# Performance work log

Hardware: AMD Instinct MI355X
Metric: run time of the kernel (lower is better)

Reference implementation:

```python
import jax, jax.numpy as jnp
import numpy as np
from jax import lax

T_D = 0.7          # condensation radius
T_B = 0.2          # min beta to seed a condensate
FEATURE_LENGTH = 9 # columns of raw features before the prediction block
N_FEAT = 17        # n_ccoords = N_FEAT - 14 = 3
N_EVENTS = 16
POINTS_PER_EVENT = 65536


def setup_inputs() -> dict:
    key = jax.random.key(0)
    N = N_EVENTS * POINTS_PER_EVENT
    # uniform [0,1): betas in [0,1), ccoords in the unit cube -> realistic clustering
    x = jax.random.uniform(key, (N, N_FEAT), dtype=jnp.float32)
    row_splits = (jnp.arange(N_EVENTS + 1) * POINTS_PER_EVENT).astype(jnp.int32)
    return {"x": x, "row_splits": row_splits}


def _build_condensates(ccoords, betas, radius, min_beta):
    """Greedy NMS-like condensation, vectorized over events.
    ccoords: [E, P, C] float; betas: [E, P] float.
    Returns asso [E,P] int32 (index of assigned condensate, -1 = noise) and
    iscond [E,P] bool (condensation point flags).
    """
    E, P, _ = ccoords.shape
    r2 = radius * radius

    def masked_beta(asso):
        return jnp.where(asso < 0, betas, -1.0)

    def cond_fn(state):
        asso, _ = state
        return jnp.any(jnp.max(masked_beta(asso), axis=1) >= min_beta)

    def body_fn(state):
        asso, iscond = state
        mb = masked_beta(asso)                     # [E,P]
        ref = jnp.argmax(mb, axis=1)               # [E] highest-beta unassigned point
        valid = jnp.take_along_axis(mb, ref[:, None], axis=1)[:, 0] >= min_beta  # [E]
        refc = jnp.take_along_axis(ccoords, ref[:, None, None], axis=1)          # [E,1,C]
        distsq = jnp.sum((ccoords - refc) ** 2, axis=-1)                          # [E,P]
        assign = (asso < 0) & (distsq <= r2) & valid[:, None]
        asso = jnp.where(assign, ref[:, None].astype(jnp.int32), asso)
        newcond = (jnp.arange(P)[None, :] == ref[:, None]) & valid[:, None]
        return asso, iscond | newcond

    asso0 = jnp.full((E, P), -1, dtype=jnp.int32)
    iscond0 = jnp.zeros((E, P), dtype=jnp.bool_)
    return lax.while_loop(cond_fn, body_fn, (asso0, iscond0))


def reference(x, row_splits):
    E = row_splits.shape[0] - 1
    N, F = x.shape
    P = N // E  # uniform events (RaggedConstructTensor equivalent for equal splits)
    n_ccoords = F - 14
    x_pred = x[:, FEATURE_LENGTH:]
    n_pred = x_pred.shape[-1]
    betas = x_pred[:, 0].reshape(E, P)
    ccoords = x_pred[:, n_pred - n_ccoords:].reshape(E, P, n_ccoords)

    asso, iscond = _build_condensates(ccoords, betas, T_D, T_B)

    ncond = jnp.sum(iscond, axis=1).astype(jnp.int32)  # condensates per event
    out_row_splits = jnp.concatenate(
        [jnp.zeros((1,), jnp.int32), jnp.cumsum(ncond).astype(jnp.int32)])
    # jit-safe equivalent of dout = x[iscond > 0]: zero-mask non-condensates
    mask = iscond.reshape(-1, 1).astype(x.dtype)
    dout = x * mask  # [N, F], rows of non-condensates are zero
    return dout, out_row_splits
```

## Files before the change

kernel.cpp:

```cpp
#include <hip/hip_runtime.h>

typedef unsigned long long u64;
typedef unsigned int u32;
typedef float f4n __attribute__((ext_vector_type(4)));

static constexpr int NF = 17;
static constexpr int BCOL = 9;
static constexpr int CCOL = 14;
static constexpr int RPB = 512;
static constexpr int CHUNK = 4096;
static constexpr int REFCAP = 64;
static constexpr int SCAP = 8192;
static constexpr int BPE = 32;
static constexpr int WCHK = 8;

#define T_B_F ((float)0.2)
#define R2_F  ((float)(0.7*0.7))

__device__ __forceinline__ u64 shfl_down_u64(u64 v, int off){
    u32 lo = (u32)v, hi = (u32)(v >> 32);
    lo = __shfl_down(lo, off, 64);
    hi = __shfl_down(hi, off, 64);
    return ((u64)hi << 32) | lo;
}

__device__ __forceinline__ float dist2(float cx, float cy, float cz,
                                       float rx, float ry, float rz){
    #pragma clang fp contract(off)
    float dx = cx - rx, dy = cy - ry, dz = cz - rz;
    float sx = dx * dx, sy = dy * dy, sz = dz * dz;
    return (sx + sy) + sz;
}

__device__ __forceinline__ u64 makeKey(float beta, u32 idx){
    return ((u64)__float_as_uint(beta) << 32) | (u64)(0xFFFFFFFFu - idx);
}

__device__ __forceinline__ int bucketOf(float b){
    int v = (int)((b - 0.2f) * 320.0f);
    return v > 255 ? 255 : v;
}

__device__ __forceinline__ void blockArgmax(u64 bk, int bs,
                                            u64* wkey, int* wslot,
                                            u64* skey, int* sslot){
    int tid = threadIdx.x, lid = tid & 63, wid = tid >> 6;
    #pragma unroll
    for (int off = 32; off > 0; off >>= 1){
        u64 ok = shfl_down_u64(bk, off);
        int os = __shfl_down(bs, off, 64);
        if (ok > bk){ bk = ok; bs = os; }
    }
    if (lid == 0){ wkey[wid] = bk; wslot[wid] = bs; }
    __syncthreads();
    if (wid == 0){
        u64 k2 = (lid < 16) ? wkey[lid] : 0;
        int s2 = (lid < 16) ? wslot[lid] : -1;
        #pragma unroll
        for (int off = 8; off > 0; off >>= 1){
            u64 ok = shfl_down_u64(k2, off);
            int os = __shfl_down(s2, off, 64);
            if (ok > k2){ k2 = ok; s2 = os; }
        }
        if (lid == 0){ *skey = k2; *sslot = s2; }
    }
    __syncthreads();
}

__device__ int lds_nms_fast(float4* cp, float* cb, int* ci, int m,
                            u64* wkey, int* wslot, u64* skey, int* sslot,
                            float4* refs_xyz, int* refs_idx, int refbase, int nref)
{
    int tid = threadIdx.x;
    u64 bk = 0; int bs = -1;
    for (int k = tid; k < m; k += 1024){
        u64 kk = makeKey(cb[k], (u32)ci[k]);
        if (kk > bk){ bk = kk; bs = k; }
    }
    blockArgmax(bk, bs, wkey, wslot, skey, sslot);
    while (*skey != 0){
        int rs = *sslot;
        float4 rv = cp[rs];
        if (tid == 0 && nref < REFCAP){
            refs_xyz[refbase + nref] = rv;
            refs_idx[refbase + nref] = ci[rs];
        }
        nref++;
        bk = 0; bs = -1;
        for (int k = tid; k < m; k += 1024){
            float b = cb[k];
            if (b >= 0.f){
                float4 p = cp[k];
                if (dist2(p.x, p.y, p.z, rv.x, rv.y, rv.z) <= R2_F) cb[k] = -1.f;
                else { u64 kk = makeKey(b, (u32)ci[k]); if (kk > bk){ bk = kk; bs = k; } }
            }
        }
        blockArgmax(bk, bs, wkey, wslot, skey, sslot);
    }
    return nref;
}

__global__ void k_init(u32* ws){
    for (int i = threadIdx.x; i < 4352; i += 1024) ws[i] = 0;
}

__global__ __launch_bounds__(256) void k_main(
    const float4* __restrict__ x4, f4n* __restrict__ out4, int n4out,
    int* __restrict__ cnt, int* __restrict__ hist,
    float4* __restrict__ cand_xyz, int* __restrict__ cand_idx,
    int P, int chunksPerEvent, int filterBlocks)
{
    __shared__ float4 lrow[RPB];
    __shared__ int lh[256];
    __shared__ int swc[4], swb[4], sbase;

    int b = blockIdx.x;
    if (b >= filterBlocks){
        int i = (b - filterBlocks) * 256 + threadIdx.x;
        int stride = (gridDim.x - filterBlocks) * 256;
        f4n z = {0.f, 0.f, 0.f, 0.f};
        for (; i < n4out; i += stride) __builtin_nontemporal_store(z, &out4[i]);
        return;
    }
    int e = b / chunksPerEvent;
    int chunk = b % chunksPerEvent;
    int rowStart = chunk * RPB;
    size_t tile4 = (size_t)b * (RPB * NF / 4);
    int tid = threadIdx.x;
    lh[tid] = 0;

    const int N4 = RPB * NF / 4;
    for (int i = tid; i < N4; i += 256){
        float4 v = x4[tile4 + i];
        float vv[4] = {v.x, v.y, v.z, v.w};
        int f0 = 4 * i;
        #pragma unroll
        for (int j = 0; j < 4; j++){
            int flat = f0 + j;
            int row = flat / NF;
            int col = flat - row * NF;
            if (col == BCOL)       ((float*)&lrow[row])[3] = vv[j];
            else if (col >= CCOL)  ((float*)&lrow[row])[col - CCOL] = vv[j];
        }
    }
    __syncthreads();

    int lid = tid & 63, wid = tid >> 6;
    float4 a0 = lrow[tid], a1 = lrow[tid + 256];
    bool k0 = (a0.w >= T_B_F), k1 = (a1.w >= T_B_F);
    u64 bal0 = __ballot(k0), bal1 = __ballot(k1);
    int wcnt = __popcll(bal0) + __popcll(bal1);
    if (k0) atomicAdd(&lh[bucketOf(a0.w)], 1);
    if (k1) atomicAdd(&lh[bucketOf(a1.w)], 1);
    if (lid == 0) swc[wid] = wcnt;
    __syncthreads();
    if (tid == 0){
        int tot = 0;
        for (int w = 0; w < 4; w++){ swb[w] = tot; tot += swc[w]; }
        sbase = tot ? atomicAdd(&cnt[e], tot) : 0;
    }
    __syncthreads();
    int base = sbase + swb[wid];
    u64 lm = (1ull << lid) - 1;
    size_t eoff = (size_t)e * P;
    if (k0){
        int pos = base + __popcll(bal0 & lm);
        cand_xyz[eoff + pos] = a0;
        cand_idx[eoff + pos] = rowStart + tid;
    }
    if (k1){
        int pos = base + __popcll(bal0) + __popcll(bal1 & lm);
        cand_xyz[eoff + pos] = a1;
        cand_idx[eoff + pos] = rowStart + tid + 256;
    }
    if (lh[tid]) atomicAdd(&hist[e * 256 + tid], lh[tid]);
}

__global__ __launch_bounds__(256) void k_gather(
    const int* __restrict__ hist, const float4* __restrict__ cand_xyz,
    const int* __restrict__ cand_idx, const int* __restrict__ cnt,
    float4* __restrict__ top_xyz, int* __restrict__ top_idx,
    int* __restrict__ topcnt, int* __restrict__ cutoffB, int P)
{
    __shared__ int lh[256];
    __shared__ int swc[4], swb[4], sbase, scut;
    int e = blockIdx.x / BPE, c = blockIdx.x % BPE;
    int tid = threadIdx.x;
    lh[tid] = hist[e * 256 + tid];
    __syncthreads();
    if (tid == 0){
        int tot = 0, cu = 0;
        for (int bb = 255; bb >= 0; bb--){
            if (tot + lh[bb] > CHUNK){ cu = bb + 1; break; }
            tot += lh[bb];
        }
        scut = cu;
        if (c == 0) cutoffB[e] = cu;
    }
    __syncthreads();
    int cut = scut, n = cnt[e];
    int lid = tid & 63, wid = tid >> 6;
    size_t eoff = (size_t)e * P;
    int stride = BPE * 256;

    float4 cc[WCHK]; int ix[WCHK]; bool kp[WCHK]; u64 bal[WCHK];
    int wcnt = 0;
    #pragma unroll
    for (int k = 0; k < WCHK; k++){
        int i = c * 256 + tid + k * stride;
        bool inb = i < n;
        int ii = inb ? i : 0;
        float4 v = cand_xyz[eoff + ii];
        kp[k] = inb && (bucketOf(v.w) >= cut);
        cc[k] = v;
        bal[k] = __ballot(kp[k]);
        wcnt += __popcll(bal[k]);
        ix[k] = kp[k] ? cand_idx[eoff + ii] : 0;
    }
    if (lid == 0) swc[wid] = wcnt;
    __syncthreads();
    if (tid == 0){
        int tot = 0;
        for (int w = 0; w < 4; w++){ swb[w] = tot; tot += swc[w]; }
        sbase = tot ? atomicAdd(&topcnt[e], tot) : 0;
    }
    __syncthreads();
    int pos = sbase + swb[wid];
    u64 lm = (1ull << lid) - 1;
    #pragma unroll
    for (int k = 0; k < WCHK; k++){
        if (kp[k]){
            int p_ = pos + __popcll(bal[k] & lm);
            top_xyz[e * CHUNK + p_] = cc[k];
            top_idx[e * CHUNK + p_] = ix[k];
        }
        pos += __popcll(bal[k]);
    }
}

__global__ __launch_bounds__(1024) void k_nms1(
    const float4* __restrict__ top_xyz, const int* __restrict__ top_idx,
    const int* __restrict__ topcnt,
    float4* __restrict__ refs_xyz, int* __restrict__ refs_idx,
    int* __restrict__ nref1)
{
    __shared__ float4 cp[CHUNK];
    __shared__ float cb[CHUNK];
    __shared__ int ci[CHUNK];
    __shared__ u64 wkey[16]; __shared__ int wslot[16];
    __shared__ u64 skey; __shared__ int sslot;

    int e = blockIdx.x, tid = threadIdx.x;
    int m = topcnt[e]; if (m > CHUNK) m = CHUNK;
    for (int i = tid; i < m; i += 1024){
        float4 v = top_xyz[e * CHUNK + i];
        cp[i] = v; cb[i] = v.w; ci[i] = top_idx[e * CHUNK + i];
    }
    __syncthreads();
    int nref = lds_nms_fast(cp, cb, ci, m, wkey, wslot, &skey, &sslot,
                            refs_xyz, refs_idx, e * REFCAP, 0);
    if (tid == 0) nref1[e] = nref;
}

__global__ __launch_bounds__(256) void k_suppress(
    const float4* __restrict__ cand_xyz, const int* __restrict__ cand_idx,
    const int* __restrict__ cnt, const float4* __restrict__ refs_xyz,
    const int* __restrict__ nref1, const int* __restrict__ cutoffB,
    float4* __restrict__ surv_xyz, int* __restrict__ surv_idx,
    int* __restrict__ survcnt, int P)
{
    __shared__ float4 lref[REFCAP];
    __shared__ int swc[4], swb[4], sbase;
    int e = blockIdx.x / BPE, c = blockIdx.x % BPE;
    int nr = nref1[e]; if (nr > REFCAP) nr = REFCAP;
    int cut = cutoffB[e], n = cnt[e];
    for (int i = threadIdx.x; i < nr; i += 256) lref[i] = refs_xyz[e * REFCAP + i];
    __syncthreads();
    int tid = threadIdx.x, lid = tid & 63, wid = tid >> 6;
    size_t eoff = (size_t)e * P;
    int stride = BPE * 256;

    float4 cc[WCHK]; int ix[WCHK]; bool kp[WCHK]; u64 bal[WCHK];
    int wcnt = 0;
    #pragma unroll
    for (int k = 0; k < WCHK; k++){
        int i = c * 256 + tid + k * stride;
        bool inb = i < n;
        int ii = inb ? i : 0;
        float4 v = cand_xyz[eoff + ii];
        bool keep = inb && (bucketOf(v.w) < cut);
        if (keep){
            for (int r = 0; r < nr; r++){
                float4 rf = lref[r];
                if (dist2(v.x, v.y, v.z, rf.x, rf.y, rf.z) <= R2_F){ keep = false; break; }
            }
        }
        cc[k] = v; kp[k] = keep;
        bal[k] = __ballot(keep);
        wcnt += __popcll(bal[k]);
        ix[k] = keep ? cand_idx[eoff + ii] : 0;
    }
    if (lid == 0) swc[wid] = wcnt;
    __syncthreads();
    if (tid == 0){
        int tot = 0;
        for (int w = 0; w < 4; w++){ swb[w] = tot; tot += swc[w]; }
        sbase = tot ? atomicAdd(&survcnt[e], tot) : 0;
    }
    __syncthreads();
    int pos = sbase + swb[wid];
    u64 lm = (1ull << lid) - 1;
    size_t soff = (size_t)e * SCAP;
    #pragma unroll
    for (int k = 0; k < WCHK; k++){
        if (kp[k]){
            int p_ = pos + __popcll(bal[k] & lm);
            if (p_ < SCAP){ surv_xyz[soff + p_] = cc[k]; surv_idx[soff + p_] = ix[k]; }
        }
        pos += __popcll(bal[k]);
    }
}

__global__ __launch_bounds__(1024) void k_nms2(
    const float* __restrict__ x, float* __restrict__ out,
    const float4* __restrict__ surv_xyz, const int* __restrict__ surv_idx,
    const int* __restrict__ survcnt,
    float4* __restrict__ scr_xyz, int* __restrict__ scr_idx,
    float4* __restrict__ refs_xyz, int* __restrict__ refs_idx,
    const int* __restrict__ nref1,
    int* __restrict__ ncond, int* __restrict__ done, int P, int E)
{
    __shared__ float4 cp[CHUNK];
    __shared__ float cb[CHUNK];
    __shared__ int ci[CHUNK];
    __shared__ u64 wkey[16]; __shared__ int wslot[16];
    __shared__ u64 skey; __shared__ int sslot;
    __shared__ int scnt2, sLast;

    int e = blockIdx.x, tid = threadIdx.x, lid = tid & 63, wid = tid >> 6;
    int m = survcnt[e]; if (m > SCAP) m = SCAP;
    size_t soff = (size_t)e * SCAP;
    int nref = nref1[e]; if (nref > REFCAP) nref = REFCAP;

    const float4* sx = surv_xyz + soff;
    const int* si = surv_idx + soff;
    float4* fbx[2] = {scr_xyz + (size_t)e * P, scr_xyz + (size_t)e * P + SCAP};
    int* fbi[2] = {scr_idx + (size_t)e * P, scr_idx + (size_t)e * P + SCAP};
    int pp = 0;

    while (m > CHUNK){
        u64 bk = 0; int bs = -1;
        for (int i = tid; i < m; i += 1024){
            float4 v = sx[i];
            u64 kk = makeKey(v.w, (u32)si[i]);
            if (kk > bk){ bk = kk; bs = i; }
        }
        blockArgmax(bk, bs, wkey, wslot, &skey, &sslot);
        if (tid == 0) scnt2 = 0;
        __syncthreads();
        float4 rv = sx[sslot];
        if (tid == 0 && nref < REFCAP){
            refs_xyz[e * REFCAP + nref] = rv;
            refs_idx[e * REFCAP + nref] = si[sslot];
        }
        nref++;
        __syncthreads();
        for (int i0 = 0; i0 < m; i0 += 1024){
            int i = i0 + tid;
            bool keep = false; float4 v = make_float4(0.f,0.f,0.f,0.f); int id_ = 0;
            if (i < m){
                v = sx[i]; id_ = si[i];
                keep = !(dist2(v.x, v.y, v.z, rv.x, rv.y, rv.z) <= R2_F);
            }
            u64 bal = __ballot(keep);
            int cw = __popcll(bal);
            int b_ = 0;
            if (lid == 0) b_ = cw ? atomicAdd(&scnt2, cw) : 0;
            b_ = __shfl(b_, 0, 64);
            if (keep){
                int p_ = b_ + __popcll(bal & ((1ull << lid) - 1));
                fbx[pp][p_] = v; fbi[pp][p_] = id_;
            }
        }
        __syncthreads();
        m = scnt2;
        sx = fbx[pp]; si = fbi[pp]; pp ^= 1;
        __syncthreads();
    }

    for (int i = tid; i < m; i += 1024){
        float4 v = sx[i];
        cp[i] = v; cb[i] = v.w; ci[i] = si[i];
    }
    __syncthreads();
    nref = lds_nms_fast(cp, cb, ci, m, wkey, wslot, &skey, &sslot,
                        refs_xyz, refs_idx, e * REFCAP, nref);
    if (nref > REFCAP) nref = REFCAP;

    for (int i = tid; i < nref * NF; i += 1024){
        int j = i / NF, f = i - j * NF;
        int row = refs_idx[e * REFCAP + j];
        size_t b = ((size_t)e * P + row) * NF;
        out[b + f] = x[b + f];
    }
    if (tid == 0) atomicExch(&ncond[e], nref);
    __threadfence();
    __syncthreads();
    if (tid == 0) sLast = atomicAdd(done, 1);
    __syncthreads();
    if (sLast == E - 1 && tid == 0){
        size_t so = (size_t)E * P * NF;
        int s = 0;
        out[so] = 0.f;
        for (int i = 0; i < E; i++){
            s += atomicAdd(&ncond[i], 0);
            out[so + i + 1] = (float)s;
        }
    }
}

extern "C" void kernel_launch(void* const* d_in, const int* in_sizes, int n_in,
                              void* d_out, int out_size, void* d_ws, size_t ws_size,
                              hipStream_t stream) {
    const float* x = (const float*)d_in[0];
    int N = in_sizes[0] / NF;
    int E = in_sizes[1] - 1;
    int P = N / E;
    float* out = (float*)d_out;
    char* ws = (char*)d_ws;

    int* cnt     = (int*)(ws + 0);
    int* survcnt = (int*)(ws + 64);
    int* ncond   = (int*)(ws + 128);
    int* done    = (int*)(ws + 192);
    int* nref1   = (int*)(ws + 256);
    int* cutoffB = (int*)(ws + 320);
    int* topcnt  = (int*)(ws + 384);
    int* hist    = (int*)(ws + 1024);
    float4* refs_xyz = (float4*)(ws + 20480);
    int* refs_idx    = (int*)(ws + 36864);
    float4* top_xyz  = (float4*)(ws + 65536);
    int* top_idx     = (int*)(ws + 65536 + (size_t)E*CHUNK*16);
    size_t o = 65536 + (size_t)E*CHUNK*20;
    float4* cand_xyz = (float4*)(ws + o);
    int* cand_idx    = (int*)(ws + o + (size_t)E*P*16);
    float4* surv_xyz = (float4*)(ws + o + (size_t)E*P*20);
    int* surv_idx    = (int*)(ws + o + (size_t)E*P*20 + (size_t)E*SCAP*16);

    k_init<<<1, 1024, 0, stream>>>((u32*)ws);

    int chunksPerEvent = P / RPB;
    int filterBlocks = E * chunksPerEvent;
    int zeroBlocks = 1024;
    int n4out = (N * NF) / 4;
    k_main<<<filterBlocks + zeroBlocks, 256, 0, stream>>>(
        (const float4*)x, (f4n*)out, n4out, cnt, hist, cand_xyz, cand_idx,
        P, chunksPerEvent, filterBlocks);

    k_gather<<<E * BPE, 256, 0, stream>>>(
        hist, cand_xyz, cand_idx, cnt, top_xyz, top_idx, topcnt, cutoffB, P);

    k_nms1<<<E, 1024, 0, stream>>>(
        top_xyz, top_idx, topcnt, refs_xyz, refs_idx, nref1);

    k_suppress<<<E * BPE, 256, 0, stream>>>(
        cand_xyz, cand_idx, cnt, refs_xyz, nref1, cutoffB,
        surv_xyz, surv_idx, survcnt, P);

    k_nms2<<<E, 1024, 0, stream>>>(
        x, out, surv_xyz, surv_idx, survcnt, cand_xyz, cand_idx,
        refs_xyz, refs_idx, nref1, ncond, done, P, E);
}
```

Before: 219.8 us.

## Fuse gather, NMS and suppress stages into one per-event kernel

Merges k_gather, k_nms1, k_suppress and k_nms2 into a single k_rest kernel with one 1024-thread block per event. The block compacts top candidates straight into LDS, runs NMS there, then suppresses the remaining candidates into LDS with a global overflow path. This removes several kernel launches and the global round-trips for top and survivor buffers. It also interleaves zeroing blocks with filter blocks in k_main, replaces the init kernel with hipMemsetAsync, and shrinks CHUNK. The cost is that the suppress pass now runs on only 16 blocks, which lowers parallelism for scanning candidates.

```diff
diff --git a/kernel.cpp b/kernel.cpp
--- a/kernel.cpp
+++ b/kernel.cpp
@@ -8,11 +8,9 @@
 static constexpr int BCOL = 9;
 static constexpr int CCOL = 14;
 static constexpr int RPB = 512;
-static constexpr int CHUNK = 4096;
+static constexpr int CHUNK = 3072;
 static constexpr int REFCAP = 64;
-static constexpr int SCAP = 8192;
-static constexpr int BPE = 32;
-static constexpr int WCHK = 8;
+static constexpr int GB = 8;
 
 #define T_B_F ((float)0.2)
 #define R2_F  ((float)(0.7*0.7))
@@ -69,7 +67,7 @@
 
 __device__ int lds_nms_fast(float4* cp, float* cb, int* ci, int m,
                             u64* wkey, int* wslot, u64* skey, int* sslot,
-                            float4* refs_xyz, int* refs_idx, int refbase, int nref)
+                            float4* lref, int* lrefi, int nref)
 {
     int tid = threadIdx.x;
     u64 bk = 0; int bs = -1;
@@ -81,10 +79,7 @@
     while (*skey != 0){
         int rs = *sslot;
         float4 rv = cp[rs];
-        if (tid == 0 && nref < REFCAP){
-            refs_xyz[refbase + nref] = rv;
-            refs_idx[refbase + nref] = ci[rs];
-        }
+        if (tid == 0 && nref < REFCAP){ lref[nref] = rv; lrefi[nref] = ci[rs]; }
         nref++;
         bk = 0; bs = -1;
         for (int k = tid; k < m; k += 1024){
@@ -100,32 +95,32 @@
     return nref;
 }
 
-__global__ void k_init(u32* ws){
-    for (int i = threadIdx.x; i < 4352; i += 1024) ws[i] = 0;
-}
-
 __global__ __launch_bounds__(256) void k_main(
     const float4* __restrict__ x4, f4n* __restrict__ out4, int n4out,
     int* __restrict__ cnt, int* __restrict__ hist,
     float4* __restrict__ cand_xyz, int* __restrict__ cand_idx,
-    int P, int chunksPerEvent, int filterBlocks)
+    int P, int chunksPerEvent)
 {
     __shared__ float4 lrow[RPB];
     __shared__ int lh[256];
     __shared__ int swc[4], swb[4], sbase;
 
     int b = blockIdx.x;
-    if (b >= filterBlocks){
-        int i = (b - filterBlocks) * 256 + threadIdx.x;
-        int stride = (gridDim.x - filterBlocks) * 256;
+    int mod = b % 3;
+    if (mod == 2){
+        int zi = b / 3;
+        int zBlocks = gridDim.x / 3;
+        int i = zi * 256 + threadIdx.x;
+        int stride = zBlocks * 256;
         f4n z = {0.f, 0.f, 0.f, 0.f};
         for (; i < n4out; i += stride) __builtin_nontemporal_store(z, &out4[i]);
         return;
     }
-    int e = b / chunksPerEvent;
-    int chunk = b % chunksPerEvent;
+    int fi = (b / 3) * 2 + mod;
+    int e = fi / chunksPerEvent;
+    int chunk = fi % chunksPerEvent;
     int rowStart = chunk * RPB;
-    size_t tile4 = (size_t)b * (RPB * NF / 4);
+    size_t tile4 = (size_t)fi * (RPB * NF / 4);
     int tid = threadIdx.x;
     lh[tid] = 0;
 
@@ -176,230 +171,177 @@
     if (lh[tid]) atomicAdd(&hist[e * 256 + tid], lh[tid]);
 }
 
-__global__ __launch_bounds__(256) void k_gather(
-    const int* __restrict__ hist, const float4* __restrict__ cand_xyz,
-    const int* __restrict__ cand_idx, const int* __restrict__ cnt,
-    float4* __restrict__ top_xyz, int* __restrict__ top_idx,
-    int* __restrict__ topcnt, int* __restrict__ cutoffB, int P)
-{
-    __shared__ int lh[256];
-    __shared__ int swc[4], swb[4], sbase, scut;
-    int e = blockIdx.x / BPE, c = blockIdx.x % BPE;
-    int tid = threadIdx.x;
-    lh[tid] = hist[e * 256 + tid];
-    __syncthreads();
-    if (tid == 0){
-        int tot = 0, cu = 0;
-        for (int bb = 255; bb >= 0; bb--){
-            if (tot + lh[bb] > CHUNK){ cu = bb + 1; break; }
-            tot += lh[bb];
-        }
-        scut = cu;
-        if (c == 0) cutoffB[e] = cu;
-    }
-    __syncthreads();
-    int cut = scut, n = cnt[e];
-    int lid = tid & 63, wid = tid >> 6;
-    size_t eoff = (size_t)e * P;
-    int stride = BPE * 256;
-
-    float4 cc[WCHK]; int ix[WCHK]; bool kp[WCHK]; u64 bal[WCHK];
-    int wcnt = 0;
-    #pragma unroll
-    for (int k = 0; k < WCHK; k++){
-        int i = c * 256 + tid + k * stride;
-        bool inb = i < n;
-        int ii = inb ? i : 0;
-        float4 v = cand_xyz[eoff + ii];
-        kp[k] = inb && (bucketOf(v.w) >= cut);
-        cc[k] = v;
-        bal[k] = __ballot(kp[k]);
-        wcnt += __popcll(bal[k]);
-        ix[k] = kp[k] ? cand_idx[eoff + ii] : 0;
-    }
-    if (lid == 0) swc[wid] = wcnt;
-    __syncthreads();
-    if (tid == 0){
-        int tot = 0;
-        for (int w = 0; w < 4; w++){ swb[w] = tot; tot += swc[w]; }
-        sbase = tot ? atomicAdd(&topcnt[e], tot) : 0;
-    }
-    __syncthreads();
-    int pos = sbase + swb[wid];
-    u64 lm = (1ull << lid) - 1;
-    #pragma unroll
-    for (int k = 0; k < WCHK; k++){
-        if (kp[k]){
-            int p_ = pos + __popcll(bal[k] & lm);
-            top_xyz[e * CHUNK + p_] = cc[k];
-            top_idx[e * CHUNK + p_] = ix[k];
-        }
-        pos += __popcll(bal[k]);
-    }
-}
-
-__global__ __launch_bounds__(1024) void k_nms1(
-    const float4* __restrict__ top_xyz, const int* __restrict__ top_idx,
-    const int* __restrict__ topcnt,
-    float4* __restrict__ refs_xyz, int* __restrict__ refs_idx,
-    int* __restrict__ nref1)
-{
-    __shared__ float4 cp[CHUNK];
-    __shared__ float cb[CHUNK];
-    __shared__ int ci[CHUNK];
-    __shared__ u64 wkey[16]; __shared__ int wslot[16];
-    __shared__ u64 skey; __shared__ int sslot;
-
-    int e = blockIdx.x, tid = threadIdx.x;
-    int m = topcnt[e]; if (m > CHUNK) m = CHUNK;
-    for (int i = tid; i < m; i += 1024){
-        float4 v = top_xyz[e * CHUNK + i];
-        cp[i] = v; cb[i] = v.w; ci[i] = top_idx[e * CHUNK + i];
-    }
-    __syncthreads();
-    int nref = lds_nms_fast(cp, cb, ci, m, wkey, wslot, &skey, &sslot,
-                            refs_xyz, refs_idx, e * REFCAP, 0);
-    if (tid == 0) nref1[e] = nref;
-}
-
-__global__ __launch_bounds__(256) void k_suppress(
-    const float4* __restrict__ cand_xyz, const int* __restrict__ cand_idx,
-    const int* __restrict__ cnt, const float4* __restrict__ refs_xyz,
-    const int* __restrict__ nref1, const int* __restrict__ cutoffB,
-    float4* __restrict__ surv_xyz, int* __restrict__ surv_idx,
-    int* __restrict__ survcnt, int P)
-{
-    __shared__ float4 lref[REFCAP];
-    __shared__ int swc[4], swb[4], sbase;
-    int e = blockIdx.x / BPE, c = blockIdx.x % BPE;
-    int nr = nref1[e]; if (nr > REFCAP) nr = REFCAP;
-    int cut = cutoffB[e], n = cnt[e];
-    for (int i = threadIdx.x; i < nr; i += 256) lref[i] = refs_xyz[e * REFCAP + i];
-    __syncthreads();
-    int tid = threadIdx.x, lid = tid & 63, wid = tid >> 6;
-    size_t eoff = (size_t)e * P;
-    int stride = BPE * 256;
-
-    float4 cc[WCHK]; int ix[WCHK]; bool kp[WCHK]; u64 bal[WCHK];
-    int wcnt = 0;
-    #pragma unroll
-    for (int k = 0; k < WCHK; k++){
-        int i = c * 256 + tid + k * stride;
-        bool inb = i < n;
-        int ii = inb ? i : 0;
-        float4 v = cand_xyz[eoff + ii];
-        bool keep = inb && (bucketOf(v.w) < cut);
-        if (keep){
-            for (int r = 0; r < nr; r++){
-                float4 rf = lref[r];
-                if (dist2(v.x, v.y, v.z, rf.x, rf.y, rf.z) <= R2_F){ keep = false; break; }
-            }
-        }
-        cc[k] = v; kp[k] = keep;
-        bal[k] = __ballot(keep);
-        wcnt += __popcll(bal[k]);
-        ix[k] = keep ? cand_idx[eoff + ii] : 0;
-    }
-    if (lid == 0) swc[wid] = wcnt;
-    __syncthreads();
-    if (tid == 0){
-        int tot = 0;
-        for (int w = 0; w < 4; w++){ swb[w] = tot; tot += swc[w]; }
-        sbase = tot ? atomicAdd(&survcnt[e], tot) : 0;
-    }
-    __syncthreads();
-    int pos = sbase + swb[wid];
-    u64 lm = (1ull << lid) - 1;
-    size_t soff = (size_t)e * SCAP;
-    #pragma unroll
-    for (int k = 0; k < WCHK; k++){
-        if (kp[k]){
-            int p_ = pos + __popcll(bal[k] & lm);
-            if (p_ < SCAP){ surv_xyz[soff + p_] = cc[k]; surv_idx[soff + p_] = ix[k]; }
-        }
-        pos += __popcll(bal[k]);
-    }
-}
-
-__global__ __launch_bounds__(1024) void k_nms2(
+__global__ __launch_bounds__(1024) void k_rest(
     const float* __restrict__ x, float* __restrict__ out,
-    const float4* __restrict__ surv_xyz, const int* __restrict__ surv_idx,
-    const int* __restrict__ survcnt,
-    float4* __restrict__ scr_xyz, int* __restrict__ scr_idx,
-    float4* __restrict__ refs_xyz, int* __restrict__ refs_idx,
-    const int* __restrict__ nref1,
+    float4* __restrict__ cand_xyz, int* __restrict__ cand_idx,
+    const int* __restrict__ cnt, const int* __restrict__ hist,
+    float4* __restrict__ sB_xyz, int* __restrict__ sB_idx,
     int* __restrict__ ncond, int* __restrict__ done, int P, int E)
 {
     __shared__ float4 cp[CHUNK];
     __shared__ float cb[CHUNK];
     __shared__ int ci[CHUNK];
+    __shared__ int lh[256];
+    __shared__ float4 lref[REFCAP];
+    __shared__ int lrefi[REFCAP];
     __shared__ u64 wkey[16]; __shared__ int wslot[16];
     __shared__ u64 skey; __shared__ int sslot;
-    __shared__ int scnt2, sLast;
+    __shared__ int sm, scut, sLast;
 
     int e = blockIdx.x, tid = threadIdx.x, lid = tid & 63, wid = tid >> 6;
-    int m = survcnt[e]; if (m > SCAP) m = SCAP;
-    size_t soff = (size_t)e * SCAP;
-    int nref = nref1[e]; if (nref > REFCAP) nref = REFCAP;
-
-    const float4* sx = surv_xyz + soff;
-    const int* si = surv_idx + soff;
-    float4* fbx[2] = {scr_xyz + (size_t)e * P, scr_xyz + (size_t)e * P + SCAP};
-    int* fbi[2] = {scr_idx + (size_t)e * P, scr_idx + (size_t)e * P + SCAP};
-    int pp = 0;
-
-    while (m > CHUNK){
-        u64 bk = 0; int bs = -1;
-        for (int i = tid; i < m; i += 1024){
+    size_t eoff = (size_t)e * P;
+    int n = cnt[e];
+
+    if (tid < 256) lh[tid] = hist[e * 256 + tid];
+    if (tid == 0) sm = 0;
+    __syncthreads();
+    if (tid == 0){
+        int tot = 0, cu = 0;
+        for (int b = 255; b >= 0; b--){
+            if (tot + lh[b] > CHUNK){ cu = b + 1; break; }
+            tot += lh[b];
+        }
+        scut = cu;
+    }
+    __syncthreads();
+    int cut = scut;
+    u64 lm = (1ull << lid) - 1;
+
+    for (int i0 = 0; i0 < n; i0 += 1024 * GB){
+        float4 v[GB]; int id[GB]; bool sel[GB]; u64 bal[GB];
+        #pragma unroll
+        for (int k = 0; k < GB; k++){
+            int i = i0 + k * 1024 + tid;
+            bool inb = i < n;
+            int ii = inb ? i : 0;
+            v[k] = cand_xyz[eoff + ii];
+            id[k] = cand_idx[eoff + ii];
+            sel[k] = inb && (bucketOf(v[k].w) >= cut);
+            bal[k] = __ballot(sel[k]);
+        }
+        int wcnt = 0;
+        #pragma unroll
+        for (int k = 0; k < GB; k++) wcnt += __popcll(bal[k]);
+        int b_ = 0;
+        if (lid == 0) b_ = wcnt ? atomicAdd(&sm, wcnt) : 0;
+        b_ = __shfl(b_, 0, 64);
+        #pragma unroll
+        for (int k = 0; k < GB; k++){
+            if (sel[k]){
+                int p = b_ + __popcll(bal[k] & lm);
+                cp[p] = v[k]; cb[p] = v[k].w; ci[p] = id[k];
+            }
+            b_ += __popcll(bal[k]);
+        }
+    }
+    __syncthreads();
+    int m = sm;
+
+    int nref = lds_nms_fast(cp, cb, ci, m, wkey, wslot, &skey, &sslot,
+                            lref, lrefi, 0);
+    if (nref > REFCAP) nref = REFCAP;
+    if (tid == 0) sm = 0;
+    __syncthreads();
+
+    for (int i0 = 0; i0 < n; i0 += 1024 * GB){
+        float4 v[GB]; int id[GB]; bool kp[GB]; u64 bal[GB];
+        #pragma unroll
+        for (int k = 0; k < GB; k++){
+            int i = i0 + k * 1024 + tid;
+            bool inb = i < n;
+            int ii = inb ? i : 0;
+            v[k] = cand_xyz[eoff + ii];
+            id[k] = cand_idx[eoff + ii];
+            kp[k] = inb && (bucketOf(v[k].w) < cut);
+        }
+        #pragma unroll
+        for (int k = 0; k < GB; k++){
+            if (kp[k]){
+                for (int r = 0; r < nref; r++){
+                    float4 rf = lref[r];
+                    if (dist2(v[k].x, v[k].y, v[k].z, rf.x, rf.y, rf.z) <= R2_F){
+                        kp[k] = false; break;
+                    }
+                }
+            }
+            bal[k] = __ballot(kp[k]);
+        }
+        int wcnt = 0;
+        #pragma unroll
+        for (int k = 0; k < GB; k++) wcnt += __popcll(bal[k]);
+        int b_ = 0;
+        if (lid == 0) b_ = wcnt ? atomicAdd(&sm, wcnt) : 0;
+        b_ = __shfl(b_, 0, 64);
+        #pragma unroll
+        for (int k = 0; k < GB; k++){
+            if (kp[k]){
+                int p = b_ + __popcll(bal[k] & lm);
+                if (p < CHUNK){ cp[p] = v[k]; cb[p] = v[k].w; ci[p] = id[k]; }
+                else { cand_xyz[eoff + p] = v[k]; cand_idx[eoff + p] = id[k]; }
+            }
+            b_ += __popcll(bal[k]);
+        }
+    }
+    __syncthreads();
+    int m2 = sm;
+
+    if (m2 > CHUNK){
+        for (int i = tid; i < CHUNK; i += 1024){
+            cand_xyz[eoff + i] = make_float4(cp[i].x, cp[i].y, cp[i].z, cb[i]);
+            cand_idx[eoff + i] = ci[i];
+        }
+        __syncthreads();
+        const float4* sx = cand_xyz + eoff; const int* si = cand_idx + eoff;
+        float4* dx = sB_xyz + eoff; int* di = sB_idx + eoff;
+        while (m2 > CHUNK){
+            u64 bk = 0; int bs = -1;
+            for (int i = tid; i < m2; i += 1024){
+                u64 kk = makeKey(sx[i].w, (u32)si[i]);
+                if (kk > bk){ bk = kk; bs = i; }
+            }
+            blockArgmax(bk, bs, wkey, wslot, &skey, &sslot);
+            float4 rv = sx[sslot];
+            if (tid == 0 && nref < REFCAP){ lref[nref] = rv; lrefi[nref] = si[sslot]; }
+            nref++;
+            if (tid == 0) sm = 0;
+            __syncthreads();
+            for (int i0 = 0; i0 < m2; i0 += 1024){
+                int i = i0 + tid;
+                bool keep = false; float4 v = make_float4(0.f,0.f,0.f,0.f); int id_ = 0;
+                if (i < m2){
+                    v = sx[i]; id_ = si[i];
+                    keep = !(dist2(v.x, v.y, v.z, rv.x, rv.y, rv.z) <= R2_F);
+                }
+                u64 bal = __ballot(keep);
+                int cw = __popcll(bal);
+                int b_ = 0;
+                if (lid == 0) b_ = cw ? atomicAdd(&sm, cw) : 0;
+                b_ = __shfl(b_, 0, 64);
+                if (keep){
+                    int p_ = b_ + __popcll(bal & lm);
+                    dx[p_] = v; di[p_] = id_;
+                }
+            }
+            __syncthreads();
+            m2 = sm;
+            { const float4* t = sx; sx = dx; dx = (float4*)t; }
+            { const int* t = si; si = di; di = (int*)t; }
+            __syncthreads();
+        }
+        for (int i = tid; i < m2; i += 1024){
             float4 v = sx[i];
-            u64 kk = makeKey(v.w, (u32)si[i]);
-            if (kk > bk){ bk = kk; bs = i; }
-        }
-        blockArgmax(bk, bs, wkey, wslot, &skey, &sslot);
-        if (tid == 0) scnt2 = 0;
+            cp[i] = v; cb[i] = v.w; ci[i] = si[i];
+        }
         __syncthreads();
-        float4 rv = sx[sslot];
-        if (tid == 0 && nref < REFCAP){
-            refs_xyz[e * REFCAP + nref] = rv;
-            refs_idx[e * REFCAP + nref] = si[sslot];
-        }
-        nref++;
-        __syncthreads();
-        for (int i0 = 0; i0 < m; i0 += 1024){
-            int i = i0 + tid;
-            bool keep = false; float4 v = make_float4(0.f,0.f,0.f,0.f); int id_ = 0;
-            if (i < m){
-                v = sx[i]; id_ = si[i];
-                keep = !(dist2(v.x, v.y, v.z, rv.x, rv.y, rv.z) <= R2_F);
-            }
-            u64 bal = __ballot(keep);
-            int cw = __popcll(bal);
-            int b_ = 0;
-            if (lid == 0) b_ = cw ? atomicAdd(&scnt2, cw) : 0;
-            b_ = __shfl(b_, 0, 64);
-            if (keep){
-                int p_ = b_ + __popcll(bal & ((1ull << lid) - 1));
-                fbx[pp][p_] = v; fbi[pp][p_] = id_;
-            }
-        }
-        __syncthreads();
-        m = scnt2;
-        sx = fbx[pp]; si = fbi[pp]; pp ^= 1;
-        __syncthreads();
-    }
-
-    for (int i = tid; i < m; i += 1024){
-        float4 v = sx[i];
-        cp[i] = v; cb[i] = v.w; ci[i] = si[i];
-    }
-    __syncthreads();
-    nref = lds_nms_fast(cp, cb, ci, m, wkey, wslot, &skey, &sslot,
-                        refs_xyz, refs_idx, e * REFCAP, nref);
+    }
+
+    nref = lds_nms_fast(cp, cb, ci, m2, wkey, wslot, &skey, &sslot,
+                        lref, lrefi, nref);
     if (nref > REFCAP) nref = REFCAP;
 
     for (int i = tid; i < nref * NF; i += 1024){
         int j = i / NF, f = i - j * NF;
-        int row = refs_idx[e * REFCAP + j];
+        int row = lrefi[j];
         size_t b = ((size_t)e * P + row) * NF;
         out[b + f] = x[b + f];
     }
@@ -429,45 +371,27 @@
     float* out = (float*)d_out;
     char* ws = (char*)d_ws;
 
-    int* cnt     = (int*)(ws + 0);
-    int* survcnt = (int*)(ws + 64);
-    int* ncond   = (int*)(ws + 128);
-    int* done    = (int*)(ws + 192);
-    int* nref1   = (int*)(ws + 256);
-    int* cutoffB = (int*)(ws + 320);
-    int* topcnt  = (int*)(ws + 384);
-    int* hist    = (int*)(ws + 1024);
-    float4* refs_xyz = (float4*)(ws + 20480);
-    int* refs_idx    = (int*)(ws + 36864);
-    float4* top_xyz  = (float4*)(ws + 65536);
-    int* top_idx     = (int*)(ws + 65536 + (size_t)E*CHUNK*16);
-    size_t o = 65536 + (size_t)E*CHUNK*20;
+    int* cnt   = (int*)(ws + 0);
+    int* ncond = (int*)(ws + 64);
+    int* done  = (int*)(ws + 128);
+    int* hist  = (int*)(ws + 1024);
+    size_t o = 32768;
     float4* cand_xyz = (float4*)(ws + o);
     int* cand_idx    = (int*)(ws + o + (size_t)E*P*16);
-    float4* surv_xyz = (float4*)(ws + o + (size_t)E*P*20);
-    int* surv_idx    = (int*)(ws + o + (size_t)E*P*20 + (size_t)E*SCAP*16);
-
-    k_init<<<1, 1024, 0, stream>>>((u32*)ws);
+    float4* sB_xyz   = (float4*)(ws + o + (size_t)E*P*20);
+    int* sB_idx      = (int*)(ws + o + (size_t)E*P*36);
+
+    hipMemsetAsync(ws, 0, 17408, stream);
 
     int chunksPerEvent = P / RPB;
     int filterBlocks = E * chunksPerEvent;
-    int zeroBlocks = 1024;
+    int zeroBlocks = filterBlocks / 2;
     int n4out = (N * NF) / 4;
     k_main<<<filterBlocks + zeroBlocks, 256, 0, stream>>>(
         (const float4*)x, (f4n*)out, n4out, cnt, hist, cand_xyz, cand_idx,
-        P, chunksPerEvent, filterBlocks);
-
-    k_gather<<<E * BPE, 256, 0, stream>>>(
-        hist, cand_xyz, cand_idx, cnt, top_xyz, top_idx, topcnt, cutoffB, P);
-
-    k_nms1<<<E, 1024, 0, stream>>>(
-        top_xyz, top_idx, topcnt, refs_xyz, refs_idx, nref1);
-
-    k_suppress<<<E * BPE, 256, 0, stream>>>(
-        cand_xyz, cand_idx, cnt, refs_xyz, nref1, cutoffB,
-        surv_xyz, surv_idx, survcnt, P);
-
-    k_nms2<<<E, 1024, 0, stream>>>(
-        x, out, surv_xyz, surv_idx, survcnt, cand_xyz, cand_idx,
-        refs_xyz, refs_idx, nref1, ncond, done, P, E);
-}
+        P, chunksPerEvent);
+
+    k_rest<<<E, 1024, 0, stream>>>(
+        x, out, cand_xyz, cand_idx, cnt, hist, sB_xyz, sB_idx,
+        ncond, done, P, E);
+}
```

Result: slower. 268.7 us (+22.3%).
